# Optimization experiments

Measured on AMD Instinct MI355X. Metric: run time of the kernel, lower is better.

Reference implementation:

```python
import jax, jax.numpy as jnp
import numpy as np
from jax import lax

SR = 44100  # sample_rate from __init__ default


def _log_scale(v, mn, mx):
    # Faithful to AudioParameter.validate_and_scale with scale='log':
    # clamp, map log(v) to [0,1] over [log(mn), log(mx)], then rescale LINEARLY to [mn, mx].
    v = float(np.clip(float(v), mn, mx))
    log_min = np.log(max(mn, 1e-6))
    log_max = np.log(mx)
    normalized = (np.log(max(v, 1e-6)) - log_min) / (log_max - log_min)
    return normalized * (mx - mn) + mn


def _eq_coeffs(frequency, gain, q, sr=SR):
    # Parameter validation/scaling (frequency, q are 'log' scale; gain is linear clamp)
    f = _log_scale(frequency, 20.0, 20000.0)
    g = float(np.clip(float(gain), -30.0, 30.0))
    Q = _log_scale(q, 0.1, 30.0)
    # torchaudio.functional.equalizer_biquad ('bell' peaking EQ) coefficients
    w0 = 2.0 * np.pi * f / sr
    A = 10.0 ** (g / 40.0)
    alpha = np.sin(w0) / (2.0 * Q)
    b0 = 1.0 + alpha * A
    b1 = -2.0 * np.cos(w0)
    b2 = 1.0 - alpha * A
    a0 = 1.0 + alpha / A
    a1 = b1
    a2 = 1.0 - alpha / A
    return (b0 / a0, b1 / a0, b2 / a0, a1 / a0, a2 / a0)


def _biquad(x, coefs):
    # Direct-form-I second-order IIR along last axis, vectorized over all leading dims.
    b0, b1, b2, a1, a2 = [jnp.asarray(c, x.dtype) for c in coefs]
    shp = x.shape
    xf = x.reshape(-1, shp[-1])  # (N, T)
    z = jnp.zeros((xf.shape[0],), x.dtype)

    def step(carry, xn):
        x1, x2, y1, y2 = carry
        yn = b0 * xn + b1 * x1 + b2 * x2 - a1 * y1 - a2 * y2
        return (xn, x1, yn, y1), yn

    _, ys = lax.scan(step, (z, z, z, z), xf.T)  # ys: (T, N)
    return ys.T.reshape(shp)


def setup_inputs() -> dict:
    key = jax.random.key(0)
    audio = jax.random.normal(key, (32, 2, 441000), dtype=jnp.float32)  # 10s stereo, batch 32
    return {"audio": audio, "frequency": 2000, "gain": 6, "q": 1}


def reference(audio, frequency, gain, q):
    # filter_type='bell' (default) -> torchaudio equalizer_biquad path
    coefs = _eq_coeffs(frequency, gain, q)
    return _biquad(audio, coefs)
```

## Files before the change

kernel.cpp:

```cpp
#include <hip/hip_runtime.h>
#include <math.h>

#ifndef M_PI
#define M_PI 3.14159265358979323846
#endif

#define T_LEN      441000
#define L          16
#define BLOCK      256
#define WARM_LANES 16
#define SEG_OUT    ((BLOCK - WARM_LANES) * L)
#define NSEG       ((T_LEN + SEG_OUT - 1) / SEG_OUT)


__device__ __forceinline__ double log_scale(double v, double mn, double mx) {
    v = fmin(fmax(v, mn), mx);
    double lmin = log(fmax(mn, 1e-6));
    double lmax = log(mx);
    double nrm = (log(fmax(v, 1e-6)) - lmin) / (lmax - lmin);
    return nrm * (mx - mn) + mn;
}

__global__ void eq_setup_kernel(const int* __restrict__ f_in,
                                const int* __restrict__ g_in,
                                const int* __restrict__ q_in,
                                float* __restrict__ ws) {
    double f = log_scale((double)f_in[0], 20.0, 20000.0);
    double g = fmin(fmax((double)g_in[0], -30.0), 30.0);
    double Q = log_scale((double)q_in[0], 0.1, 30.0);
    double w0 = 2.0 * M_PI * f / 44100.0;
    double A  = pow(10.0, g / 40.0);
    double al = sin(w0) / (2.0 * Q);
    double ca = cos(w0);
    double b0 = 1.0 + al * A;
    double b1 = -2.0 * ca;
    double b2 = 1.0 - al * A;
    double a0 = 1.0 + al / A;
    double B0 = b0 / a0, B1 = b1 / a0, B2 = b2 / a0;
    double A1 = b1 / a0, A2 = (1.0 - al / A) / a0;
    ws[0] = (float)B0; ws[1] = (float)B1; ws[2] = (float)B2;
    ws[3] = (float)A1; ws[4] = (float)A2;

    double p11 = -A1, p12 = -A2, p21 = 1.0, p22 = 0.0;
    for (int i = 0; i < 4; ++i) {
        double s11 = p11 * p11 + p12 * p21;
        double s12 = p11 * p12 + p12 * p22;
        double s21 = p21 * p11 + p22 * p21;
        double s22 = p21 * p12 + p22 * p22;
        p11 = s11; p12 = s12; p21 = s21; p22 = s22;
    }
    for (int j = 0; j < 7; ++j) {
        ws[5 + 4 * j + 0] = (float)p11;
        ws[5 + 4 * j + 1] = (float)p12;
        ws[5 + 4 * j + 2] = (float)p21;
        ws[5 + 4 * j + 3] = (float)p22;
        double s11 = p11 * p11 + p12 * p21;
        double s12 = p11 * p12 + p12 * p22;
        double s21 = p21 * p11 + p22 * p21;
        double s22 = p21 * p12 + p22 * p22;
        p11 = s11; p12 = s12; p21 = s21; p22 = s22;
    }
}

__global__ __launch_bounds__(BLOCK, 4) void eq_main_kernel(
        const float* __restrict__ x,
        const float* __restrict__ ws,
        float* __restrict__ y) {
    const int tid  = threadIdx.x;
    const int lane = tid & 63;
    const int wv   = tid >> 6;
    const int ch   = blockIdx.y;

    const float b0 = ws[0], b1 = ws[1], b2 = ws[2], a1 = ws[3], a2 = ws[4];

    const float* __restrict__ xc = x + (size_t)ch * T_LEN;
    float*       __restrict__ yc = y + (size_t)ch * T_LEN;

    const int w0   = blockIdx.x * SEG_OUT - WARM_LANES * L;
    const int base = w0 + tid * L;

    float xv[L], xm1, xm2;
    if (base >= 2 && base + L <= T_LEN) {
        const float4 v0 = *reinterpret_cast<const float4*>(xc + base + 0);
        const float4 v1 = *reinterpret_cast<const float4*>(xc + base + 4);
        const float4 v2 = *reinterpret_cast<const float4*>(xc + base + 8);
        const float4 v3 = *reinterpret_cast<const float4*>(xc + base + 12);
        xv[0]=v0.x; xv[1]=v0.y; xv[2]=v0.z; xv[3]=v0.w;
        xv[4]=v1.x; xv[5]=v1.y; xv[6]=v1.z; xv[7]=v1.w;
        xv[8]=v2.x; xv[9]=v2.y; xv[10]=v2.z; xv[11]=v2.w;
        xv[12]=v3.x; xv[13]=v3.y; xv[14]=v3.z; xv[15]=v3.w;
        xm1 = xc[base - 1];
        xm2 = xc[base - 2];
    } else {
#pragma unroll
        for (int k = 0; k < L; ++k) {
            const int idx = base + k;
            xv[k] = (idx >= 0 && idx < T_LEN) ? xc[idx] : 0.f;
        }
        xm1 = (base - 1 >= 0 && base - 1 < T_LEN) ? xc[base - 1] : 0.f;
        xm2 = (base - 2 >= 0 && base - 2 < T_LEN) ? xc[base - 2] : 0.f;
    }

    float t[L];
    t[0] = fmaf(b0, xv[0], fmaf(b1, xm1, b2 * xm2));
    t[1] = fmaf(b0, xv[1], fmaf(b1, xv[0], b2 * xm1));
#pragma unroll
    for (int k = 2; k < L; ++k)
        t[k] = fmaf(b0, xv[k], fmaf(b1, xv[k - 1], b2 * xv[k - 2]));

    float c0 = 0.f, c1 = 0.f;
#pragma unroll
    for (int k = 0; k < L; ++k) {
        const float yn = fmaf(-a1, c0, fmaf(-a2, c1, t[k]));
        c1 = c0; c0 = yn;
    }
    const float l0 = c0, l1 = c1;

#pragma unroll
    for (int j = 0; j < 6; ++j) {
        const float m11 = ws[5 + 4 * j + 0], m12 = ws[5 + 4 * j + 1];
        const float m21 = ws[5 + 4 * j + 2], m22 = ws[5 + 4 * j + 3];
        const float d0 = __shfl_up(c0, 1u << j);
        const float d1 = __shfl_up(c1, 1u << j);
        if (lane >= (1 << j)) {
            c0 = fmaf(m11, d0, fmaf(m12, d1, c0));
            c1 = fmaf(m21, d0, fmaf(m22, d1, c1));
        }
    }

    __shared__ float wsum[BLOCK / 64][2];
    if (lane == 63) { wsum[wv][0] = c0; wsum[wv][1] = c1; }
    __syncthreads();
    const float A11 = ws[5 + 24 + 0], A12 = ws[5 + 24 + 1];
    const float A21 = ws[5 + 24 + 2], A22 = ws[5 + 24 + 3];
    float g0 = 0.f, g1 = 0.f;
    for (int w = 0; w < wv; ++w) {
        const float n0 = fmaf(A11, g0, fmaf(A12, g1, wsum[w][0]));
        const float n1 = fmaf(A21, g0, fmaf(A22, g1, wsum[w][1]));
        g0 = n0; g1 = n1;
    }

    c0 = l0; c1 = l1;
    if (lane == 0) {
        const float m11 = ws[5], m12 = ws[6], m21 = ws[7], m22 = ws[8];
        c0 = fmaf(m11, g0, fmaf(m12, g1, l0));
        c1 = fmaf(m21, g0, fmaf(m22, g1, l1));
    }
#pragma unroll
    for (int j = 0; j < 6; ++j) {
        const float m11 = ws[5 + 4 * j + 0], m12 = ws[5 + 4 * j + 1];
        const float m21 = ws[5 + 4 * j + 2], m22 = ws[5 + 4 * j + 3];
        const float d0 = __shfl_up(c0, 1u << j);
        const float d1 = __shfl_up(c1, 1u << j);
        if (lane >= (1 << j)) {
            c0 = fmaf(m11, d0, fmaf(m12, d1, c0));
            c1 = fmaf(m21, d0, fmaf(m22, d1, c1));
        }
    }
    float s0 = __shfl_up(c0, 1);
    float s1 = __shfl_up(c1, 1);
    if (lane == 0) { s0 = g0; s1 = g1; }

    float yv[L];
    float p0 = s0, p1 = s1;
#pragma unroll
    for (int k = 0; k < L; ++k) {
        const float yn = fmaf(-a1, p0, fmaf(-a2, p1, t[k]));
        p1 = p0; p0 = yn;
        yv[k] = yn;
    }

    if (tid >= WARM_LANES && base < T_LEN) {
        if (base + L <= T_LEN) {
            *reinterpret_cast<float4*>(yc + base + 0)  = make_float4(yv[0], yv[1], yv[2], yv[3]);
            *reinterpret_cast<float4*>(yc + base + 4)  = make_float4(yv[4], yv[5], yv[6], yv[7]);
            *reinterpret_cast<float4*>(yc + base + 8)  = make_float4(yv[8], yv[9], yv[10], yv[11]);
            *reinterpret_cast<float4*>(yc + base + 12) = make_float4(yv[12], yv[13], yv[14], yv[15]);
        } else {
#pragma unroll
            for (int k = 0; k < L; ++k)
                if (base + k < T_LEN) yc[base + k] = yv[k];
        }
    }
}

extern "C" void kernel_launch(void* const* d_in, const int* in_sizes, int n_in,
                              void* d_out, int out_size, void* d_ws, size_t ws_size,
                              hipStream_t stream) {
    const float* x = (const float*)d_in[0];
    const int*   f = (const int*)d_in[1];
    const int*   g = (const int*)d_in[2];
    const int*   q = (const int*)d_in[3];
    float*       y  = (float*)d_out;
    float*       ws = (float*)d_ws;

    eq_setup_kernel<<<1, 1, 0, stream>>>(f, g, q, ws);

    const int nch = in_sizes[0] / T_LEN;
    dim3 grid(NSEG, nch);
    eq_main_kernel<<<grid, dim3(BLOCK), 0, stream>>>(x, ws, y);
}
```

Measured before the change: 210.7 us.

## Make each wavefront an independent segment, dropping cross-wave scan and barrier

Each 64-lane wavefront now handles its own output segment, warmed up by 8 discarded lanes, so the shared-memory cross-wave combine and __syncthreads are gone. The per-thread chunk grows from 16 to 32 samples and the filter matrix powers are recomputed for the new chunk length. Output stores become nontemporal, and the FIR stage is computed in place to save registers. In exchange, the warm-up is a truncation of the IIR state that relies on the filter's impulse response decaying within 256 samples, and the warm-up overhead is now about 14% of the work instead of 6%.

```diff
diff --git a/kernel.cpp b/kernel.cpp
--- a/kernel.cpp
+++ b/kernel.cpp
@@ -6,11 +6,16 @@
 #endif
 
 #define T_LEN      441000
-#define L          16
-#define BLOCK      256
-#define WARM_LANES 16
-#define SEG_OUT    ((BLOCK - WARM_LANES) * L)
-#define NSEG       ((T_LEN + SEG_OUT - 1) / SEG_OUT)
+#define L          32
+#define WARM_LANES 8
+#define OUT_LANES  (64 - WARM_LANES)
+#define SEG_OUT    (OUT_LANES * L)
+#define WPC        ((T_LEN + SEG_OUT - 1) / SEG_OUT)
+#define WVB        4
+#define BLOCK      (WVB * 64)
+#define GX         ((WPC + WVB - 1) / WVB)
+
+typedef float vfloat4 __attribute__((ext_vector_type(4)));
 
 
 __device__ __forceinline__ double log_scale(double v, double mn, double mx) {
@@ -36,20 +41,21 @@
     double b1 = -2.0 * ca;
     double b2 = 1.0 - al * A;
     double a0 = 1.0 + al / A;
-    double B0 = b0 / a0, B1 = b1 / a0, B2 = b2 / a0;
-    double A1 = b1 / a0, A2 = (1.0 - al / A) / a0;
-    ws[0] = (float)B0; ws[1] = (float)B1; ws[2] = (float)B2;
-    ws[3] = (float)A1; ws[4] = (float)A2;
+    ws[0] = (float)(b0 / a0);
+    ws[1] = (float)(b1 / a0);
+    ws[2] = (float)(b2 / a0);
+    ws[3] = (float)(b1 / a0);
+    ws[4] = (float)((1.0 - al / A) / a0);
 
-    double p11 = -A1, p12 = -A2, p21 = 1.0, p22 = 0.0;
-    for (int i = 0; i < 4; ++i) {
+    double p11 = -(b1 / a0), p12 = -((1.0 - al / A) / a0), p21 = 1.0, p22 = 0.0;
+    for (int i = 0; i < 5; ++i) {
         double s11 = p11 * p11 + p12 * p21;
         double s12 = p11 * p12 + p12 * p22;
         double s21 = p21 * p11 + p22 * p21;
         double s22 = p21 * p12 + p22 * p22;
         p11 = s11; p12 = s12; p21 = s21; p22 = s22;
     }
-    for (int j = 0; j < 7; ++j) {
+    for (int j = 0; j < 6; ++j) {
         ws[5 + 4 * j + 0] = (float)p11;
         ws[5 + 4 * j + 1] = (float)p12;
         ws[5 + 4 * j + 2] = (float)p21;
@@ -62,33 +68,28 @@
     }
 }
 
-__global__ __launch_bounds__(BLOCK, 4) void eq_main_kernel(
+__global__ __launch_bounds__(BLOCK, 6) void eq_main_kernel(
         const float* __restrict__ x,
         const float* __restrict__ ws,
         float* __restrict__ y) {
-    const int tid  = threadIdx.x;
-    const int lane = tid & 63;
-    const int wv   = tid >> 6;
-    const int ch   = blockIdx.y;
+    const int lane = threadIdx.x & 63;
+    const int wvg  = blockIdx.x * WVB + (threadIdx.x >> 6);
+    if (wvg >= WPC) return;
 
-    const float b0 = ws[0], b1 = ws[1], b2 = ws[2], a1 = ws[3], a2 = ws[4];
-
+    const int ch = blockIdx.y;
     const float* __restrict__ xc = x + (size_t)ch * T_LEN;
     float*       __restrict__ yc = y + (size_t)ch * T_LEN;
 
-    const int w0   = blockIdx.x * SEG_OUT - WARM_LANES * L;
-    const int base = w0 + tid * L;
+    const int start = wvg * SEG_OUT - WARM_LANES * L;
+    const int base  = start + lane * L;
 
     float xv[L], xm1, xm2;
     if (base >= 2 && base + L <= T_LEN) {
-        const float4 v0 = *reinterpret_cast<const float4*>(xc + base + 0);
-        const float4 v1 = *reinterpret_cast<const float4*>(xc + base + 4);
-        const float4 v2 = *reinterpret_cast<const float4*>(xc + base + 8);
-        const float4 v3 = *reinterpret_cast<const float4*>(xc + base + 12);
-        xv[0]=v0.x; xv[1]=v0.y; xv[2]=v0.z; xv[3]=v0.w;
-        xv[4]=v1.x; xv[5]=v1.y; xv[6]=v1.z; xv[7]=v1.w;
-        xv[8]=v2.x; xv[9]=v2.y; xv[10]=v2.z; xv[11]=v2.w;
-        xv[12]=v3.x; xv[13]=v3.y; xv[14]=v3.z; xv[15]=v3.w;
+#pragma unroll
+        for (int k = 0; k < L; k += 4) {
+            const vfloat4 v = *reinterpret_cast<const vfloat4*>(xc + base + k);
+            xv[k] = v.x; xv[k + 1] = v.y; xv[k + 2] = v.z; xv[k + 3] = v.w;
+        }
         xm1 = xc[base - 1];
         xm2 = xc[base - 2];
     } else {
@@ -101,51 +102,21 @@
         xm2 = (base - 2 >= 0 && base - 2 < T_LEN) ? xc[base - 2] : 0.f;
     }
 
-    float t[L];
-    t[0] = fmaf(b0, xv[0], fmaf(b1, xm1, b2 * xm2));
-    t[1] = fmaf(b0, xv[1], fmaf(b1, xv[0], b2 * xm1));
+    const float b0 = ws[0], b1 = ws[1], b2 = ws[2], a1 = ws[3], a2 = ws[4];
+
 #pragma unroll
-    for (int k = 2; k < L; ++k)
-        t[k] = fmaf(b0, xv[k], fmaf(b1, xv[k - 1], b2 * xv[k - 2]));
+    for (int k = L - 1; k >= 2; --k)
+        xv[k] = fmaf(b0, xv[k], fmaf(b1, xv[k - 1], b2 * xv[k - 2]));
+    xv[1] = fmaf(b0, xv[1], fmaf(b1, xv[0], b2 * xm1));
+    xv[0] = fmaf(b0, xv[0], fmaf(b1, xm1, b2 * xm2));
 
     float c0 = 0.f, c1 = 0.f;
 #pragma unroll
     for (int k = 0; k < L; ++k) {
-        const float yn = fmaf(-a1, c0, fmaf(-a2, c1, t[k]));
+        const float yn = fmaf(-a1, c0, fmaf(-a2, c1, xv[k]));
         c1 = c0; c0 = yn;
     }
-    const float l0 = c0, l1 = c1;
 
-#pragma unroll
-    for (int j = 0; j < 6; ++j) {
-        const float m11 = ws[5 + 4 * j + 0], m12 = ws[5 + 4 * j + 1];
-        const float m21 = ws[5 + 4 * j + 2], m22 = ws[5 + 4 * j + 3];
-        const float d0 = __shfl_up(c0, 1u << j);
-        const float d1 = __shfl_up(c1, 1u << j);
-        if (lane >= (1 << j)) {
-            c0 = fmaf(m11, d0, fmaf(m12, d1, c0));
-            c1 = fmaf(m21, d0, fmaf(m22, d1, c1));
-        }
-    }
-
-    __shared__ float wsum[BLOCK / 64][2];
-    if (lane == 63) { wsum[wv][0] = c0; wsum[wv][1] = c1; }
-    __syncthreads();
-    const float A11 = ws[5 + 24 + 0], A12 = ws[5 + 24 + 1];
-    const float A21 = ws[5 + 24 + 2], A22 = ws[5 + 24 + 3];
-    float g0 = 0.f, g1 = 0.f;
-    for (int w = 0; w < wv; ++w) {
-        const float n0 = fmaf(A11, g0, fmaf(A12, g1, wsum[w][0]));
-        const float n1 = fmaf(A21, g0, fmaf(A22, g1, wsum[w][1]));
-        g0 = n0; g1 = n1;
-    }
-
-    c0 = l0; c1 = l1;
-    if (lane == 0) {
-        const float m11 = ws[5], m12 = ws[6], m21 = ws[7], m22 = ws[8];
-        c0 = fmaf(m11, g0, fmaf(m12, g1, l0));
-        c1 = fmaf(m21, g0, fmaf(m22, g1, l1));
-    }
 #pragma unroll
     for (int j = 0; j < 6; ++j) {
         const float m11 = ws[5 + 4 * j + 0], m12 = ws[5 + 4 * j + 1];
@@ -159,27 +130,28 @@
     }
     float s0 = __shfl_up(c0, 1);
     float s1 = __shfl_up(c1, 1);
-    if (lane == 0) { s0 = g0; s1 = g1; }
+    if (lane == 0) { s0 = 0.f; s1 = 0.f; }
 
-    float yv[L];
     float p0 = s0, p1 = s1;
 #pragma unroll
     for (int k = 0; k < L; ++k) {
-        const float yn = fmaf(-a1, p0, fmaf(-a2, p1, t[k]));
+        const float yn = fmaf(-a1, p0, fmaf(-a2, p1, xv[k]));
         p1 = p0; p0 = yn;
-        yv[k] = yn;
+        xv[k] = yn;
     }
 
-    if (tid >= WARM_LANES && base < T_LEN) {
+    if (lane >= WARM_LANES && base < T_LEN) {
         if (base + L <= T_LEN) {
-            *reinterpret_cast<float4*>(yc + base + 0)  = make_float4(yv[0], yv[1], yv[2], yv[3]);
-            *reinterpret_cast<float4*>(yc + base + 4)  = make_float4(yv[4], yv[5], yv[6], yv[7]);
-            *reinterpret_cast<float4*>(yc + base + 8)  = make_float4(yv[8], yv[9], yv[10], yv[11]);
-            *reinterpret_cast<float4*>(yc + base + 12) = make_float4(yv[12], yv[13], yv[14], yv[15]);
+#pragma unroll
+            for (int k = 0; k < L; k += 4) {
+                vfloat4 o;
+                o.x = xv[k]; o.y = xv[k + 1]; o.z = xv[k + 2]; o.w = xv[k + 3];
+                __builtin_nontemporal_store(o, reinterpret_cast<vfloat4*>(yc + base + k));
+            }
         } else {
 #pragma unroll
             for (int k = 0; k < L; ++k)
-                if (base + k < T_LEN) yc[base + k] = yv[k];
+                if (base + k < T_LEN) yc[base + k] = xv[k];
         }
     }
 }
@@ -197,6 +169,6 @@
     eq_setup_kernel<<<1, 1, 0, stream>>>(f, g, q, ws);
 
     const int nch = in_sizes[0] / T_LEN;
-    dim3 grid(NSEG, nch);
+    dim3 grid(GX, nch);
     eq_main_kernel<<<grid, dim3(BLOCK), 0, stream>>>(x, ws, y);
 }
```

Result: slower. 320.1 us (+51.9%).
